# Performance work log

Measured on AMD Instinct MI355X. Metric: run time of the kernel, lower is better.

The kernel has to match this reference:

```python
import jax, jax.numpy as jnp
import numpy as np

D_MODEL = 1024
NUM_HEADS = 16
HEAD_DIM = D_MODEL // NUM_HEADS
B, T = 2, 2048


def setup_inputs() -> dict:
    key = jax.random.key(0)
    kx, kq, kk, kv, ko = jax.random.split(key, 5)
    s = 1.0 / np.sqrt(D_MODEL)  # ~Linear init scale
    return {
        "x": jax.random.normal(kx, (B, T, D_MODEL), dtype=jnp.float32),
        "Wq": jax.random.normal(kq, (D_MODEL, D_MODEL), dtype=jnp.float32) * s,
        "Wk": jax.random.normal(kk, (D_MODEL, D_MODEL), dtype=jnp.float32) * s,
        "Wv": jax.random.normal(kv, (D_MODEL, D_MODEL), dtype=jnp.float32) * s,
        "Wo": jax.random.normal(ko, (D_MODEL, D_MODEL), dtype=jnp.float32) * s,
    }


def reference(x, Wq, Wk, Wv, Wo):
    Bc, Tc, _ = x.shape
    H, D = NUM_HEADS, HEAD_DIM
    scale = jnp.sqrt(jnp.asarray(D, x.dtype))
    # torch Linear (bias=False): y = x @ W^T
    q = (x @ Wq.T).reshape(Bc, Tc, H, D).transpose(0, 2, 1, 3)  # [B,H,T,D]
    k = (x @ Wk.T).reshape(Bc, Tc, H, D).transpose(0, 2, 1, 3)
    v = (x @ Wv.T).reshape(Bc, Tc, H, D).transpose(0, 2, 1, 3)
    scores = jnp.einsum("bhtd,bhsd->bhts", q, k) / scale  # [B,H,T,T]
    # causal bias: upper triangle (strictly future positions) gets -1e9
    causal_bias = jnp.triu(jnp.ones((Tc, Tc), dtype=jnp.float32), k=1) * -1e9
    scores = scores + causal_bias
    weights = jax.nn.softmax(scores, axis=-1)
    # dropout is identity in eval / p=0
    out = jnp.einsum("bhts,bhsd->bhtd", weights, v)  # [B,H,T,D]
    out = out.transpose(0, 2, 1, 3).reshape(Bc, Tc, H * D)
    return out @ Wo.T
```

## Files before the change

### kernel.cpp

```cpp
#include <hip/hip_runtime.h>
#include <hip/hip_bf16.h>

typedef __bf16 bf16_t;
typedef __bf16 bf16x2 __attribute__((ext_vector_type(2)));
typedef __bf16 bf16x4 __attribute__((ext_vector_type(4)));
typedef __bf16 bf16x8 __attribute__((ext_vector_type(8)));
typedef float  f32x4  __attribute__((ext_vector_type(4)));

#define D_MODEL 1024
#define HEADS   16
#define HD      64
#define BB      2
#define TT      2048
#define MROWS   (BB*TT)

#define GLDS16(g, l) __builtin_amdgcn_global_load_lds( \
    (const __attribute__((address_space(1))) void*)(g), \
    (__attribute__((address_space(3))) void*)(l), 16, 0, 0)

static __device__ __forceinline__ int pack_bf16(float a, float b) {
    bf16x2 t; t[0] = (bf16_t)a; t[1] = (bf16_t)b;
    return __builtin_bit_cast(int, t);
}

__global__ __launch_bounds__(256) void cvt_all_kernel(const float* __restrict__ x,
                                                      const float* __restrict__ wq,
                                                      const float* __restrict__ wk,
                                                      const float* __restrict__ wv,
                                                      const float* __restrict__ wo,
                                                      bf16_t* __restrict__ dst) {
    const int i = blockIdx.x * 256 + threadIdx.x;
    const float* src;
    int s;
    if (i < 1048576) { src = x; s = i; }
    else {
        int j = i - 1048576;
        int w = j >> 18;
        s = j & 262143;
        src = (w == 0) ? wq : (w == 1) ? wk : (w == 2) ? wv : wo;
    }
    float4 v = reinterpret_cast<const float4*>(src)[s];
    bf16x4 o;
    o[0] = (bf16_t)v.x; o[1] = (bf16_t)v.y; o[2] = (bf16_t)v.z; o[3] = (bf16_t)v.w;
    reinterpret_cast<bf16x4*>(dst)[i] = o;
}

template<int MODE, int BN>
__global__ __launch_bounds__(256) void gemm_bt(const bf16_t* __restrict__ A,
                                               const bf16_t* __restrict__ Bw,
                                               void* __restrict__ Cout,
                                               int M, int N, int K) {
    constexpr int NI = BN / 32;
    __shared__ __align__(16) bf16_t As[128*32];
    __shared__ __align__(16) bf16_t Bs[BN*32];
    const int tid   = threadIdx.x;
    const int lane  = tid & 63;
    const int wave  = tid >> 6;
    const int col16 = lane & 15;
    const int quad  = lane >> 4;
    const int wrow  = (wave & 1) * 64;
    const int wcol  = (wave >> 1) * (BN / 2);
    const int bm    = blockIdx.y * 128;
    const int bn    = blockIdx.x * BN;

    const int lr = tid >> 2;
    const int lc = (tid & 3) * 8;

    const bf16_t* agp = &A [(size_t)(bm + lr)*K + lc];
    const bf16_t* bgp = &Bw[(size_t)(bn + lr)*K + lc];
    const size_t half = (size_t)64 * K;
    bf16_t* as_lo = &As[wave*512];
    bf16_t* as_hi = &As[2048 + wave*512];
    bf16_t* bs_lo = &Bs[wave*512];
    bf16_t* bs_hi = &Bs[2048 + wave*512];

    f32x4 acc[4][NI];
#pragma unroll
    for (int i = 0; i < 4; i++)
#pragma unroll
        for (int j = 0; j < NI; j++) acc[i][j] = (f32x4){0.f, 0.f, 0.f, 0.f};

    for (int k0 = 0; k0 < K; k0 += 32) {
        GLDS16(agp + k0,        as_lo);
        GLDS16(agp + half + k0, as_hi);
        GLDS16(bgp + k0,        bs_lo);
        if (BN == 128) GLDS16(bgp + half + k0, bs_hi);
        __syncthreads();

        bf16x8 af[4], bfr[NI];
#pragma unroll
        for (int mi = 0; mi < 4; mi++)
            af[mi] = *reinterpret_cast<const bf16x8*>(&As[(wrow + mi*16 + col16)*32 + quad*8]);
#pragma unroll
        for (int ni = 0; ni < NI; ni++)
            bfr[ni] = *reinterpret_cast<const bf16x8*>(&Bs[(wcol + ni*16 + col16)*32 + quad*8]);
#pragma unroll
        for (int mi = 0; mi < 4; mi++)
#pragma unroll
            for (int ni = 0; ni < NI; ni++)
                acc[mi][ni] = __builtin_amdgcn_mfma_f32_16x16x32_bf16(af[mi], bfr[ni], acc[mi][ni], 0, 0, 0);
        __syncthreads();
    }

#pragma unroll
    for (int mi = 0; mi < 4; mi++) {
#pragma unroll
        for (int r = 0; r < 4; r++) {
            const int gm = bm + wrow + mi*16 + quad*4 + r;
            const int t  = gm & (TT - 1);
            const int b  = gm >> 11;
#pragma unroll
            for (int ni = 0; ni < NI; ni++) {
                const int gn = bn + wcol + ni*16 + col16;
                const float v = acc[mi][ni][r];
                if (MODE == 2) {
                    reinterpret_cast<float*>(Cout)[(size_t)gm * N + gn] = v;
                } else {
                    const int which = gn >> 10;
                    const int n = gn & 1023;
                    const int h = n >> 6, d = n & 63;
                    const size_t off = (size_t)(which == 2 ? 3 : which) * MROWS * D_MODEL;
                    bf16_t* base = reinterpret_cast<bf16_t*>(Cout) + off;
                    base[(((size_t)(b*HEADS + h))*TT + t)*HD + d] = (bf16_t)v;
                }
            }
        }
    }
}

__global__ __launch_bounds__(256) void transpose_v(const bf16_t* __restrict__ V,
                                                   bf16_t* __restrict__ Vt) {
    __shared__ bf16_t tile[64][72];
    const int tid = threadIdx.x;
    const int bh = blockIdx.y;
    const int t0 = blockIdx.x * 64;
    const bf16_t* src = V + ((size_t)bh * TT + t0) * HD;
#pragma unroll
    for (int i = 0; i < 2; i++) {
        const int r = i*32 + (tid >> 3), c = (tid & 7) * 8;
        *reinterpret_cast<bf16x8*>(&tile[r][c]) =
            *reinterpret_cast<const bf16x8*>(&src[(size_t)r * HD + c]);
    }
    __syncthreads();
    bf16_t* dst = Vt + (size_t)bh * HD * TT + t0;
#pragma unroll
    for (int i = 0; i < 2; i++) {
        const int d = i*32 + (tid >> 3), tc = (tid & 7) * 8;
        bf16x8 o;
#pragma unroll
        for (int j = 0; j < 8; j++) o[j] = tile[tc + j][d];
        *reinterpret_cast<bf16x8*>(&dst[(size_t)d * TT + tc]) = o;
    }
}

__global__ __launch_bounds__(256, 5) void attn_kernel(const bf16_t* __restrict__ Q,
                                                      const bf16_t* __restrict__ Kk,
                                                      const bf16_t* __restrict__ Vt,
                                                      bf16_t* __restrict__ O) {
    __shared__ __align__(16) bf16_t Ks[2][64*64];
    __shared__ __align__(16) bf16_t Vs[2][64*64];

    const int tid   = threadIdx.x;
    const int lane  = tid & 63;
    const int wave  = tid >> 6;
    const int col16 = lane & 15;
    const int quad  = lane >> 4;

    const int bx = blockIdx.x;
    const int r_ = bx >> 8, s_ = bx & 255;
    const int bh = s_ & 31;
    const int qt = (r_ == 0) ? (24 + (s_ >> 5))
                             : ((r_ - 1) * 8 + 7 - (s_ >> 5));
    const int qb    = qt * 64;
    const int qbase = qb + wave * 16;
    const int nkt   = qt + 1;

    const bf16_t* Qb = Q  + (size_t)bh * TT * HD;
    const bf16_t* Kb = Kk + (size_t)bh * TT * HD;
    const bf16_t* Vb = Vt + (size_t)bh * HD * TT;

    bf16x8 qf0 = *reinterpret_cast<const bf16x8*>(&Qb[(size_t)(qbase + col16)*HD + quad*8]);
    bf16x8 qf1 = *reinterpret_cast<const bf16x8*>(&Qb[(size_t)(qbase + col16)*HD + 32 + quad*8]);

    const int srow = (tid >> 3) & 31;
    const int sg   = ((lane & 7) ^ (srow & 7)) * 8;

    auto stage = [&](int kt, int buf) {
        const int s0 = kt * 64;
        GLDS16(&Kb[(size_t)(s0 + srow)*HD + sg],        &Ks[buf][wave*512]);
        GLDS16(&Kb[(size_t)(s0 + srow + 32)*HD + sg],   &Ks[buf][2048 + wave*512]);
        GLDS16(&Vb[(size_t)srow*TT + s0 + sg],          &Vs[buf][wave*512]);
        GLDS16(&Vb[(size_t)(srow + 32)*TT + s0 + sg],   &Vs[buf][2048 + wave*512]);
    };

    f32x4 acc[4];
#pragma unroll
    for (int i = 0; i < 4; i++) acc[i] = (f32x4){0.f,0.f,0.f,0.f};
    float lsum = 0.f;

    const float sc = 0.125f * 1.4426950408889634f;
    const int x7 = col16 & 7;
    const int a1 = ((quad & 1) * 32 + col16) * 4;
    const int a2 = a1 + 64;
    const bool hi = quad >= 2;

    stage(0, 0);
    __syncthreads();

    for (int kt = 0; kt < nkt; kt++) {
        const int buf = kt & 1;
        if (kt + 1 < nkt) stage(kt + 1, buf ^ 1);
        const int s0 = kt * 64;
        const bool diag = (kt == nkt - 1);

        int pk[4][2];
#pragma unroll
        for (int c = 0; c < 4; c++) {
            bf16x8 k0 = *reinterpret_cast<const bf16x8*>(
                &Ks[buf][(c*16 + col16)*64 + ((0*4 + quad) ^ x7)*8]);
            bf16x8 k1 = *reinterpret_cast<const bf16x8*>(
                &Ks[buf][(c*16 + col16)*64 + ((1*4 + quad) ^ x7)*8]);
            f32x4 sv = __builtin_amdgcn_mfma_f32_16x16x32_bf16(k0, qf0, (f32x4){0.f,0.f,0.f,0.f}, 0, 0, 0);
            sv       = __builtin_amdgcn_mfma_f32_16x16x32_bf16(k1, qf1, sv, 0, 0, 0);

            float pr[4];
#pragma unroll
            for (int r = 0; r < 4; r++) pr[r] = exp2f(sv[r] * sc);
            if (diag) {
#pragma unroll
                for (int r = 0; r < 4; r++)
                    if (s0 + c*16 + quad*4 + r > qbase + col16) pr[r] = 0.f;
            }
#pragma unroll
            for (int r = 0; r < 4; r++) lsum += pr[r];
            pk[c][0] = pack_bf16(pr[0], pr[1]);
            pk[c][1] = pack_bf16(pr[2], pr[3]);
        }

#pragma unroll
        for (int kc = 0; kc < 2; kc++) {
            int b0l = __builtin_amdgcn_ds_bpermute(a1, pk[2*kc][0]);
            int b0h = __builtin_amdgcn_ds_bpermute(a1, pk[2*kc+1][0]);
            int b1l = __builtin_amdgcn_ds_bpermute(a1, pk[2*kc][1]);
            int b1h = __builtin_amdgcn_ds_bpermute(a1, pk[2*kc+1][1]);
            int b2l = __builtin_amdgcn_ds_bpermute(a2, pk[2*kc][0]);
            int b2h = __builtin_amdgcn_ds_bpermute(a2, pk[2*kc+1][0]);
            int b3l = __builtin_amdgcn_ds_bpermute(a2, pk[2*kc][1]);
            int b3h = __builtin_amdgcn_ds_bpermute(a2, pk[2*kc+1][1]);
            int4 bi = { hi ? b0h : b0l, hi ? b1h : b1l, hi ? b2h : b2l, hi ? b3h : b3l };
            bf16x8 pf = __builtin_bit_cast(bf16x8, bi);
#pragma unroll
            for (int c = 0; c < 4; c++) {
                bf16x8 vf = *reinterpret_cast<const bf16x8*>(
                    &Vs[buf][(c*16 + col16)*64 + ((kc*4 + quad) ^ x7)*8]);
                acc[c] = __builtin_amdgcn_mfma_f32_16x16x32_bf16(vf, pf, acc[c], 0, 0, 0);
            }
        }
        __syncthreads();
    }

    float l = lsum;
    l += __shfl_xor(l, 16);
    l += __shfl_xor(l, 32);
    const float inv = 1.0f / l;

    const int b_ = bh >> 4, h = bh & 15;
    const int t = qbase + col16;
    bf16_t* Ob = &O[(((size_t)(b_*TT + t))*HEADS + h)*HD + quad*4];
#pragma unroll
    for (int c = 0; c < 4; c++) {
        bf16x4 o4;
#pragma unroll
        for (int r = 0; r < 4; r++) o4[r] = (bf16_t)(acc[c][r] * inv);
        *reinterpret_cast<bf16x4*>(&Ob[c*16]) = o4;
    }
}

extern "C" void kernel_launch(void* const* d_in, const int* in_sizes, int n_in,
                              void* d_out, int out_size, void* d_ws, size_t ws_size,
                              hipStream_t stream) {
    const float* x  = (const float*)d_in[0];
    const float* Wq = (const float*)d_in[1];
    const float* Wk = (const float*)d_in[2];
    const float* Wv = (const float*)d_in[3];
    const float* Wo = (const float*)d_in[4];
    float* out = (float*)d_out;

    bf16_t* Xb  = (bf16_t*)d_ws;
    bf16_t* Wqb = Xb  + (size_t)MROWS * D_MODEL;
    bf16_t* Wob = Wqb + (size_t)3 * D_MODEL * D_MODEL;
    bf16_t* Qw  = Wob + (size_t)D_MODEL * D_MODEL;
    bf16_t* Kw  = Qw  + (size_t)MROWS * D_MODEL;
    bf16_t* Vt  = Kw  + (size_t)MROWS * D_MODEL;
    bf16_t* Ow  = Vt  + (size_t)MROWS * D_MODEL;

    cvt_all_kernel<<<(MROWS*D_MODEL + 4*D_MODEL*D_MODEL) / 4 / 256, 256, 0, stream>>>(
        x, Wq, Wk, Wv, Wo, Xb);

    dim3 gqkv(3 * D_MODEL / 128, MROWS / 128);
    gemm_bt<0,128><<<gqkv, 256, 0, stream>>>(Xb, Wqb, Qw, MROWS, 3 * D_MODEL, D_MODEL);

    dim3 gt(TT / 64, BB * HEADS);
    transpose_v<<<gt, 256, 0, stream>>>(Ow, Vt);

    attn_kernel<<<dim3(1024), 256, 0, stream>>>(Qw, Kw, Vt, Ow);

    dim3 go(D_MODEL / 64, MROWS / 128);
    gemm_bt<2,64><<<go, 256, 0, stream>>>(Ow, Wob, out, MROWS, D_MODEL, D_MODEL);
}
```

Baseline: 193.3 us.

## Process 128-query tiles per attention block and fold softmax scale into Q

Each attention block now handles 128 query rows, with each wave covering 32 rows as two 16-row groups. Each K/V tile staged in shared memory is therefore reused for twice as many MFMAs, and the grid is halved. The softmax scale times log2(e) moves into the QKV GEMM epilogue for Q, which removes a multiply per score. Waves skip key tiles entirely above the causal diagonal. The cost is more registers, with launch bounds lowered from 5 to 2, fewer blocks for load balance, and slightly different rounding from pre-scaling Q in bf16.

```diff
diff --git a/kernel.cpp b/kernel.cpp
--- a/kernel.cpp
+++ b/kernel.cpp
@@ -112,11 +112,12 @@
 #pragma unroll
             for (int ni = 0; ni < NI; ni++) {
                 const int gn = bn + wcol + ni*16 + col16;
-                const float v = acc[mi][ni][r];
+                float v = acc[mi][ni][r];
                 if (MODE == 2) {
                     reinterpret_cast<float*>(Cout)[(size_t)gm * N + gn] = v;
                 } else {
                     const int which = gn >> 10;
+                    if (which == 0) v *= 0.18033688f;
                     const int n = gn & 1023;
                     const int h = n >> 6, d = n & 63;
                     const size_t off = (size_t)(which == 2 ? 3 : which) * MROWS * D_MODEL;
@@ -153,7 +154,7 @@
     }
 }
 
-__global__ __launch_bounds__(256, 5) void attn_kernel(const bf16_t* __restrict__ Q,
+__global__ __launch_bounds__(256, 2) void attn_kernel(const bf16_t* __restrict__ Q,
                                                       const bf16_t* __restrict__ Kk,
                                                       const bf16_t* __restrict__ Vt,
                                                       bf16_t* __restrict__ O) {
@@ -169,18 +170,22 @@
     const int bx = blockIdx.x;
     const int r_ = bx >> 8, s_ = bx & 255;
     const int bh = s_ & 31;
-    const int qt = (r_ == 0) ? (24 + (s_ >> 5))
-                             : ((r_ - 1) * 8 + 7 - (s_ >> 5));
-    const int qb    = qt * 64;
-    const int qbase = qb + wave * 16;
-    const int nkt   = qt + 1;
+    const int qt = (r_ == 0) ? (8 + (s_ >> 5)) : (7 - (s_ >> 5));
+    const int qb    = qt * 128;
+    const int qwave = qb + wave * 32;
+    const int nkt   = 2 * qt + 2;
 
     const bf16_t* Qb = Q  + (size_t)bh * TT * HD;
     const bf16_t* Kb = Kk + (size_t)bh * TT * HD;
     const bf16_t* Vb = Vt + (size_t)bh * HD * TT;
 
-    bf16x8 qf0 = *reinterpret_cast<const bf16x8*>(&Qb[(size_t)(qbase + col16)*HD + quad*8]);
-    bf16x8 qf1 = *reinterpret_cast<const bf16x8*>(&Qb[(size_t)(qbase + col16)*HD + 32 + quad*8]);
+    bf16x8 qf[2][2];
+#pragma unroll
+    for (int g = 0; g < 2; g++) {
+        const bf16_t* qp = &Qb[(size_t)(qwave + g*16 + col16)*HD + quad*8];
+        qf[g][0] = *reinterpret_cast<const bf16x8*>(qp);
+        qf[g][1] = *reinterpret_cast<const bf16x8*>(qp + 32);
+    }
 
     const int srow = (tid >> 3) & 31;
     const int sg   = ((lane & 7) ^ (srow & 7)) * 8;
@@ -193,12 +198,13 @@
         GLDS16(&Vb[(size_t)(srow + 32)*TT + s0 + sg],   &Vs[buf][2048 + wave*512]);
     };
 
-    f32x4 acc[4];
-#pragma unroll
-    for (int i = 0; i < 4; i++) acc[i] = (f32x4){0.f,0.f,0.f,0.f};
-    float lsum = 0.f;
-
-    const float sc = 0.125f * 1.4426950408889634f;
+    f32x4 acc[2][4];
+    float lsum[2] = {0.f, 0.f};
+#pragma unroll
+    for (int g = 0; g < 2; g++)
+#pragma unroll
+        for (int i = 0; i < 4; i++) acc[g][i] = (f32x4){0.f,0.f,0.f,0.f};
+
     const int x7 = col16 & 7;
     const int a1 = ((quad & 1) * 32 + col16) * 4;
     const int a2 = a1 + 64;
@@ -211,68 +217,80 @@
         const int buf = kt & 1;
         if (kt + 1 < nkt) stage(kt + 1, buf ^ 1);
         const int s0 = kt * 64;
-        const bool diag = (kt == nkt - 1);
-
-        int pk[4][2];
-#pragma unroll
-        for (int c = 0; c < 4; c++) {
-            bf16x8 k0 = *reinterpret_cast<const bf16x8*>(
-                &Ks[buf][(c*16 + col16)*64 + ((0*4 + quad) ^ x7)*8]);
-            bf16x8 k1 = *reinterpret_cast<const bf16x8*>(
-                &Ks[buf][(c*16 + col16)*64 + ((1*4 + quad) ^ x7)*8]);
-            f32x4 sv = __builtin_amdgcn_mfma_f32_16x16x32_bf16(k0, qf0, (f32x4){0.f,0.f,0.f,0.f}, 0, 0, 0);
-            sv       = __builtin_amdgcn_mfma_f32_16x16x32_bf16(k1, qf1, sv, 0, 0, 0);
-
-            float pr[4];
-#pragma unroll
-            for (int r = 0; r < 4; r++) pr[r] = exp2f(sv[r] * sc);
-            if (diag) {
-#pragma unroll
-                for (int r = 0; r < 4; r++)
-                    if (s0 + c*16 + quad*4 + r > qbase + col16) pr[r] = 0.f;
+
+        if (s0 <= qwave + 31) {
+            int pk[2][4][2];
+#pragma unroll
+            for (int c = 0; c < 4; c++) {
+                bf16x8 k0 = *reinterpret_cast<const bf16x8*>(
+                    &Ks[buf][(c*16 + col16)*64 + ((0*4 + quad) ^ x7)*8]);
+                bf16x8 k1 = *reinterpret_cast<const bf16x8*>(
+                    &Ks[buf][(c*16 + col16)*64 + ((1*4 + quad) ^ x7)*8]);
+#pragma unroll
+                for (int g = 0; g < 2; g++) {
+                    f32x4 sv = __builtin_amdgcn_mfma_f32_16x16x32_bf16(k0, qf[g][0],
+                                   (f32x4){0.f,0.f,0.f,0.f}, 0, 0, 0);
+                    sv       = __builtin_amdgcn_mfma_f32_16x16x32_bf16(k1, qf[g][1], sv, 0, 0, 0);
+
+                    const int qg = qwave + g*16;
+                    float pr[4];
+#pragma unroll
+                    for (int r = 0; r < 4; r++) pr[r] = exp2f(sv[r]);
+                    if (s0 + 63 > qg) {
+#pragma unroll
+                        for (int r = 0; r < 4; r++)
+                            if (s0 + c*16 + quad*4 + r > qg + col16) pr[r] = 0.f;
+                    }
+                    lsum[g] += (pr[0] + pr[1]) + (pr[2] + pr[3]);
+                    pk[g][c][0] = pack_bf16(pr[0], pr[1]);
+                    pk[g][c][1] = pack_bf16(pr[2], pr[3]);
+                }
             }
-#pragma unroll
-            for (int r = 0; r < 4; r++) lsum += pr[r];
-            pk[c][0] = pack_bf16(pr[0], pr[1]);
-            pk[c][1] = pack_bf16(pr[2], pr[3]);
-        }
-
-#pragma unroll
-        for (int kc = 0; kc < 2; kc++) {
-            int b0l = __builtin_amdgcn_ds_bpermute(a1, pk[2*kc][0]);
-            int b0h = __builtin_amdgcn_ds_bpermute(a1, pk[2*kc+1][0]);
-            int b1l = __builtin_amdgcn_ds_bpermute(a1, pk[2*kc][1]);
-            int b1h = __builtin_amdgcn_ds_bpermute(a1, pk[2*kc+1][1]);
-            int b2l = __builtin_amdgcn_ds_bpermute(a2, pk[2*kc][0]);
-            int b2h = __builtin_amdgcn_ds_bpermute(a2, pk[2*kc+1][0]);
-            int b3l = __builtin_amdgcn_ds_bpermute(a2, pk[2*kc][1]);
-            int b3h = __builtin_amdgcn_ds_bpermute(a2, pk[2*kc+1][1]);
-            int4 bi = { hi ? b0h : b0l, hi ? b1h : b1l, hi ? b2h : b2l, hi ? b3h : b3l };
-            bf16x8 pf = __builtin_bit_cast(bf16x8, bi);
-#pragma unroll
-            for (int c = 0; c < 4; c++) {
-                bf16x8 vf = *reinterpret_cast<const bf16x8*>(
-                    &Vs[buf][(c*16 + col16)*64 + ((kc*4 + quad) ^ x7)*8]);
-                acc[c] = __builtin_amdgcn_mfma_f32_16x16x32_bf16(vf, pf, acc[c], 0, 0, 0);
+
+#pragma unroll
+            for (int kc = 0; kc < 2; kc++) {
+                bf16x8 pf[2];
+#pragma unroll
+                for (int g = 0; g < 2; g++) {
+                    int b0l = __builtin_amdgcn_ds_bpermute(a1, pk[g][2*kc][0]);
+                    int b0h = __builtin_amdgcn_ds_bpermute(a1, pk[g][2*kc+1][0]);
+                    int b1l = __builtin_amdgcn_ds_bpermute(a1, pk[g][2*kc][1]);
+                    int b1h = __builtin_amdgcn_ds_bpermute(a1, pk[g][2*kc+1][1]);
+                    int b2l = __builtin_amdgcn_ds_bpermute(a2, pk[g][2*kc][0]);
+                    int b2h = __builtin_amdgcn_ds_bpermute(a2, pk[g][2*kc+1][0]);
+                    int b3l = __builtin_amdgcn_ds_bpermute(a2, pk[g][2*kc][1]);
+                    int b3h = __builtin_amdgcn_ds_bpermute(a2, pk[g][2*kc+1][1]);
+                    int4 bi = { hi ? b0h : b0l, hi ? b1h : b1l, hi ? b2h : b2l, hi ? b3h : b3l };
+                    pf[g] = __builtin_bit_cast(bf16x8, bi);
+                }
+#pragma unroll
+                for (int c = 0; c < 4; c++) {
+                    bf16x8 vf = *reinterpret_cast<const bf16x8*>(
+                        &Vs[buf][(c*16 + col16)*64 + ((kc*4 + quad) ^ x7)*8]);
+                    acc[0][c] = __builtin_amdgcn_mfma_f32_16x16x32_bf16(vf, pf[0], acc[0][c], 0, 0, 0);
+                    acc[1][c] = __builtin_amdgcn_mfma_f32_16x16x32_bf16(vf, pf[1], acc[1][c], 0, 0, 0);
+                }
             }
         }
         __syncthreads();
     }
 
-    float l = lsum;
-    l += __shfl_xor(l, 16);
-    l += __shfl_xor(l, 32);
-    const float inv = 1.0f / l;
-
     const int b_ = bh >> 4, h = bh & 15;
-    const int t = qbase + col16;
-    bf16_t* Ob = &O[(((size_t)(b_*TT + t))*HEADS + h)*HD + quad*4];
-#pragma unroll
-    for (int c = 0; c < 4; c++) {
-        bf16x4 o4;
-#pragma unroll
-        for (int r = 0; r < 4; r++) o4[r] = (bf16_t)(acc[c][r] * inv);
-        *reinterpret_cast<bf16x4*>(&Ob[c*16]) = o4;
+#pragma unroll
+    for (int g = 0; g < 2; g++) {
+        float l = lsum[g];
+        l += __shfl_xor(l, 16);
+        l += __shfl_xor(l, 32);
+        const float inv = 1.0f / l;
+        const int t = qwave + g*16 + col16;
+        bf16_t* Ob = &O[(((size_t)(b_*TT + t))*HEADS + h)*HD + quad*4];
+#pragma unroll
+        for (int c = 0; c < 4; c++) {
+            bf16x4 o4;
+#pragma unroll
+            for (int r = 0; r < 4; r++) o4[r] = (bf16_t)(acc[g][c][r] * inv);
+            *reinterpret_cast<bf16x4*>(&Ob[c*16]) = o4;
+        }
     }
 }
 
@@ -303,7 +321,7 @@
     dim3 gt(TT / 64, BB * HEADS);
     transpose_v<<<gt, 256, 0, stream>>>(Ow, Vt);
 
-    attn_kernel<<<dim3(1024), 256, 0, stream>>>(Qw, Kw, Vt, Ow);
+    attn_kernel<<<dim3(512), 256, 0, stream>>>(Qw, Kw, Vt, Ow);
 
     dim3 go(D_MODEL / 64, MROWS / 128);
     gemm_bt<2,64><<<go, 256, 0, stream>>>(Ow, Wob, out, MROWS, D_MODEL, D_MODEL);
```

Result: slower. 213.4 us (+10.4%).

## Split long causal attention rows across KV halves with atomic combine

Applied to the files above, without the earlier changes.

Query tiles in the upper half of the sequence now have their key range split into two blocks (keys 0-15 and 16-qt), each accumulating unnormalized output and row sums into fp32 buffers via atomics. A combine kernel then normalizes those rows. Short rows still write directly. The softmax scale is folded into Q in the QKV GEMM epilogue. The aim is to balance per-block work and raise parallelism. The cost is a memset, many fp32 atomics, and an extra kernel, with the accumulators reusing the workspace region that held Xb.

```diff
diff --git a/kernel.cpp b/kernel.cpp
--- a/kernel.cpp
+++ b/kernel.cpp
@@ -112,11 +112,12 @@
 #pragma unroll
             for (int ni = 0; ni < NI; ni++) {
                 const int gn = bn + wcol + ni*16 + col16;
-                const float v = acc[mi][ni][r];
+                float v = acc[mi][ni][r];
                 if (MODE == 2) {
                     reinterpret_cast<float*>(Cout)[(size_t)gm * N + gn] = v;
                 } else {
                     const int which = gn >> 10;
+                    if (which == 0) v *= 0.18033688f;
                     const int n = gn & 1023;
                     const int h = n >> 6, d = n & 63;
                     const size_t off = (size_t)(which == 2 ? 3 : which) * MROWS * D_MODEL;
@@ -156,7 +157,9 @@
 __global__ __launch_bounds__(256, 5) void attn_kernel(const bf16_t* __restrict__ Q,
                                                       const bf16_t* __restrict__ Kk,
                                                       const bf16_t* __restrict__ Vt,
-                                                      bf16_t* __restrict__ O) {
+                                                      bf16_t* __restrict__ O,
+                                                      float* __restrict__ Oacc,
+                                                      float* __restrict__ Lacc) {
     __shared__ __align__(16) bf16_t Ks[2][64*64];
     __shared__ __align__(16) bf16_t Vs[2][64*64];
 
@@ -167,13 +170,18 @@
     const int quad  = lane >> 4;
 
     const int bx = blockIdx.x;
-    const int r_ = bx >> 8, s_ = bx & 255;
-    const int bh = s_ & 31;
-    const int qt = (r_ == 0) ? (24 + (s_ >> 5))
-                             : ((r_ - 1) * 8 + 7 - (s_ >> 5));
+    int bh, qt, kbeg, kend;
+    bool direct;
+    if (bx < 512) {
+        bh = bx & 31; qt = 16 + (bx >> 5); kbeg = 0; kend = 16; direct = false;
+    } else {
+        const int j = bx - 512, w = j >> 5;
+        bh = j & 31;
+        if ((w & 1) == 0) { qt = 31 - (w >> 1); kbeg = 16; kend = qt + 1; direct = false; }
+        else              { qt = 15 - (w >> 1); kbeg = 0;  kend = qt + 1; direct = true;  }
+    }
     const int qb    = qt * 64;
     const int qbase = qb + wave * 16;
-    const int nkt   = qt + 1;
 
     const bf16_t* Qb = Q  + (size_t)bh * TT * HD;
     const bf16_t* Kb = Kk + (size_t)bh * TT * HD;
@@ -198,20 +206,19 @@
     for (int i = 0; i < 4; i++) acc[i] = (f32x4){0.f,0.f,0.f,0.f};
     float lsum = 0.f;
 
-    const float sc = 0.125f * 1.4426950408889634f;
     const int x7 = col16 & 7;
     const int a1 = ((quad & 1) * 32 + col16) * 4;
     const int a2 = a1 + 64;
     const bool hi = quad >= 2;
 
-    stage(0, 0);
+    stage(kbeg, 0);
     __syncthreads();
 
-    for (int kt = 0; kt < nkt; kt++) {
-        const int buf = kt & 1;
-        if (kt + 1 < nkt) stage(kt + 1, buf ^ 1);
+    for (int kt = kbeg; kt < kend; kt++) {
+        const int buf = (kt - kbeg) & 1;
+        if (kt + 1 < kend) stage(kt + 1, buf ^ 1);
         const int s0 = kt * 64;
-        const bool diag = (kt == nkt - 1);
+        const bool diag = (kt == qt);
 
         int pk[4][2];
 #pragma unroll
@@ -225,14 +232,13 @@
 
             float pr[4];
 #pragma unroll
-            for (int r = 0; r < 4; r++) pr[r] = exp2f(sv[r] * sc);
+            for (int r = 0; r < 4; r++) pr[r] = exp2f(sv[r]);
             if (diag) {
 #pragma unroll
                 for (int r = 0; r < 4; r++)
                     if (s0 + c*16 + quad*4 + r > qbase + col16) pr[r] = 0.f;
             }
-#pragma unroll
-            for (int r = 0; r < 4; r++) lsum += pr[r];
+            lsum += (pr[0] + pr[1]) + (pr[2] + pr[3]);
             pk[c][0] = pack_bf16(pr[0], pr[1]);
             pk[c][1] = pack_bf16(pr[2], pr[3]);
         }
@@ -259,21 +265,50 @@
         __syncthreads();
     }
 
-    float l = lsum;
-    l += __shfl_xor(l, 16);
-    l += __shfl_xor(l, 32);
-    const float inv = 1.0f / l;
-
-    const int b_ = bh >> 4, h = bh & 15;
-    const int t = qbase + col16;
-    bf16_t* Ob = &O[(((size_t)(b_*TT + t))*HEADS + h)*HD + quad*4];
-#pragma unroll
-    for (int c = 0; c < 4; c++) {
-        bf16x4 o4;
-#pragma unroll
-        for (int r = 0; r < 4; r++) o4[r] = (bf16_t)(acc[c][r] * inv);
-        *reinterpret_cast<bf16x4*>(&Ob[c*16]) = o4;
-    }
+    if (direct) {
+        float l = lsum;
+        l += __shfl_xor(l, 16);
+        l += __shfl_xor(l, 32);
+        const float inv = 1.0f / l;
+        const int b_ = bh >> 4, h = bh & 15;
+        const int t = qbase + col16;
+        bf16_t* Ob = &O[(((size_t)(b_*TT + t))*HEADS + h)*HD + quad*4];
+#pragma unroll
+        for (int c = 0; c < 4; c++) {
+            bf16x4 o4;
+#pragma unroll
+            for (int r = 0; r < 4; r++) o4[r] = (bf16_t)(acc[c][r] * inv);
+            *reinterpret_cast<bf16x4*>(&Ob[c*16]) = o4;
+        }
+    } else {
+        float l = lsum;
+        l += __shfl_xor(l, 16);
+        l += __shfl_xor(l, 32);
+        const int tq = qbase + col16 - 1024;
+        if (lane < 16) atomicAdd(&Lacc[bh*1024 + tq], l);
+        float* Op = &Oacc[((size_t)(bh*1024 + tq))*64 + quad*4];
+#pragma unroll
+        for (int c = 0; c < 4; c++)
+#pragma unroll
+            for (int r = 0; r < 4; r++)
+                atomicAdd(&Op[c*16 + r], acc[c][r]);
+    }
+}
+
+__global__ __launch_bounds__(256) void combine_kernel(const float* __restrict__ Oacc,
+                                                      const float* __restrict__ Lacc,
+                                                      bf16_t* __restrict__ O) {
+    const int i = (blockIdx.x * 256 + threadIdx.x) * 4;
+    const int bhtq = i >> 6;
+    const int d = i & 63;
+    const int bh = bhtq >> 10, tq = bhtq & 1023;
+    const float inv = 1.0f / Lacc[bhtq];
+    float4 v = *reinterpret_cast<const float4*>(&Oacc[i]);
+    bf16x4 o;
+    o[0] = (bf16_t)(v.x * inv); o[1] = (bf16_t)(v.y * inv);
+    o[2] = (bf16_t)(v.z * inv); o[3] = (bf16_t)(v.w * inv);
+    const int b = bh >> 4, h = bh & 15, t = 1024 + tq;
+    *reinterpret_cast<bf16x4*>(&O[(((size_t)(b*TT + t))*HEADS + h)*HD + d]) = o;
 }
 
 extern "C" void kernel_launch(void* const* d_in, const int* in_sizes, int n_in,
@@ -293,6 +328,8 @@
     bf16_t* Kw  = Qw  + (size_t)MROWS * D_MODEL;
     bf16_t* Vt  = Kw  + (size_t)MROWS * D_MODEL;
     bf16_t* Ow  = Vt  + (size_t)MROWS * D_MODEL;
+    float*  Oacc = (float*)d_ws;
+    float*  Lacc = (float*)((char*)d_ws + (size_t)8*1024*1024);
 
     cvt_all_kernel<<<(MROWS*D_MODEL + 4*D_MODEL*D_MODEL) / 4 / 256, 256, 0, stream>>>(
         x, Wq, Wk, Wv, Wo, Xb);
@@ -303,7 +340,11 @@
     dim3 gt(TT / 64, BB * HEADS);
     transpose_v<<<gt, 256, 0, stream>>>(Ow, Vt);
 
-    attn_kernel<<<dim3(1024), 256, 0, stream>>>(Qw, Kw, Vt, Ow);
+    hipMemsetAsync(d_ws, 0, (size_t)8*1024*1024 + 128*1024, stream);
+
+    attn_kernel<<<dim3(1536), 256, 0, stream>>>(Qw, Kw, Vt, Ow, Oacc, Lacc);
+
+    combine_kernel<<<dim3(2048), 256, 0, stream>>>(Oacc, Lacc, Ow);
 
     dim3 go(D_MODEL / 64, MROWS / 128);
     gemm_bt<2,64><<<go, 256, 0, stream>>>(Ow, Wob, out, MROWS, D_MODEL, D_MODEL);
```

New measurement: 237.6 us. 1.23x slower.
